# Performance work log

Measured on AMD Instinct MI355X. Metric: run time of the kernel, lower is better.

Reference implementation:

```python
import jax, jax.numpy as jnp
import numpy as np

B, L, D, I = 64, 196, 2048, 512

def setup_inputs() -> dict:
    key = jax.random.key(0)
    ks = jax.random.split(key, 8)
    s_f = 1.0 / np.sqrt(D)
    s_h = 1.0 / np.sqrt(I)
    s_a = 1.0 / np.sqrt(I)
    return {
        "feature_vectors": jax.random.normal(ks[0], (B, L, D), dtype=jnp.float32),
        "hidden_state": jax.random.normal(ks[1], (B, I), dtype=jnp.float32),
        "W_f": jax.random.uniform(ks[2], (D, I), jnp.float32, -s_f, s_f),
        "b_f": jax.random.uniform(ks[3], (I,), jnp.float32, -s_f, s_f),
        "W_h": jax.random.uniform(ks[4], (I, I), jnp.float32, -s_h, s_h),
        "b_h": jax.random.uniform(ks[5], (I,), jnp.float32, -s_h, s_h),
        "W_a": jax.random.uniform(ks[6], (I, D), jnp.float32, -s_a, s_a),
        "b_a": jax.random.uniform(ks[7], (D,), jnp.float32, -s_a, s_a),
    }

def reference(feature_vectors, hidden_state, W_f, b_f, W_h, b_h, W_a, b_a):
    # fv: [B,L,D], hidden: [B,I]
    fv_shaped = jnp.einsum('bld,di->bli', feature_vectors, W_f) + b_f      # [B,L,I]
    hs_shaped = hidden_state @ W_h + b_h                                   # [B,I]
    e = jnp.einsum('bli,id->bld', fv_shaped + hs_shaped[:, None, :], W_a) + b_a  # [B,L,D]
    alpha = jax.nn.softmax(e, axis=1)                                      # softmax over L locations
    z = jnp.sum(alpha * feature_vectors, axis=1)                           # [B,D] (vectorized loop)
    return (z, alpha)
```

## Files before the change

kernel.cpp:

```cpp
#include <hip/hip_runtime.h>

#define B_ 64
#define L_ 196
#define D_ 2048
#define I_ 512
#define M_ (B_*L_)

typedef __attribute__((ext_vector_type(8))) short bf16x8;
typedef __attribute__((ext_vector_type(4))) float f32x4;
typedef unsigned short u16;

__device__ __forceinline__ u16 f2bf(float x){
  unsigned u = __float_as_uint(x);
  u += 0x7fffu + ((u >> 16) & 1u);
  return (u16)(u >> 16);
}

__device__ __forceinline__ void gld16(const void* g, void* l){
  __builtin_amdgcn_global_load_lds(
      (const __attribute__((address_space(1))) void*)g,
      (__attribute__((address_space(3))) void*)l, 16, 0, 0);
}

template<int N> __device__ __forceinline__ void wait_vm(){
  __builtin_amdgcn_s_waitcnt((N&15) | ((N&48)<<10) | (7<<4) | (15<<8));
}
__device__ __forceinline__ void wait_lgkm0(){
  __builtin_amdgcn_s_waitcnt(15 | (48<<10) | (7<<4));
}
__device__ __forceinline__ void bar(){
  asm volatile("" ::: "memory");
  __builtin_amdgcn_s_barrier();
  asm volatile("" ::: "memory");
}

__global__ void transpose_cvt_kernel(const float* __restrict__ in, u16* __restrict__ out, int R, int C){
  __shared__ float tile[32][33];
  int c0 = blockIdx.x*32, r0 = blockIdx.y*32;
  int tx = threadIdx.x, ty = threadIdx.y;
  for (int i=0;i<32;i+=8)
    tile[ty+i][tx] = in[(size_t)(r0+ty+i)*C + c0 + tx];
  __syncthreads();
  for (int i=0;i<32;i+=8)
    out[(size_t)(c0+ty+i)*R + r0 + tx] = f2bf(tile[tx][ty+i]);
}

__launch_bounds__(256)
__global__ void hs_kernel(const float* __restrict__ hidden, const float* __restrict__ Wh,
                          const float* __restrict__ bh, float* __restrict__ hs){
  __shared__ float red[4][64];
  const int nl = threadIdx.x & 63, kg = threadIdx.x >> 6;
  const int n = blockIdx.x*64 + nl, b = blockIdx.y;
  const float* hrow = hidden + b*I_;
  float a0=0.f, a1=0.f;
  #pragma unroll
  for (int k=kg*128; k<kg*128+128; k+=2){
    a0 = fmaf(hrow[k+0], Wh[(size_t)(k+0)*I_ + n], a0);
    a1 = fmaf(hrow[k+1], Wh[(size_t)(k+1)*I_ + n], a1);
  }
  red[kg][nl] = a0 + a1;
  __syncthreads();
  if (kg == 0)
    hs[b*I_ + n] = bh[n] + (red[0][nl]+red[1][nl]) + (red[2][nl]+red[3][nl]);
}

__launch_bounds__(256)
__global__ void gemm1_kernel(const float* __restrict__ A, const u16* __restrict__ Bt,
                             const float* __restrict__ bias, const float* __restrict__ hs,
                             u16* __restrict__ outb)
{
  constexpr int K = D_, BK = 32, NIT = K/BK;
  __shared__ __align__(16) float Als[2][64*32];
  __shared__ __align__(16) u16  Bls[2][64*32];

  const int tid = threadIdx.x, lane = tid&63, wave = tid>>6;
  const int lid = blockIdx.y*8 + blockIdx.x;
  const int wid = (lid & 7)*196 + (lid >> 3);
  const int m0 = (wid >> 3)*64, n0 = (wid & 7)*64;
  const int q = lane>>4, mr = lane&15;
  const int wrow = (wave&1)*32, wcol = (wave>>1)*32;

  const int arow = lane>>3, achk = (lane&7)^arow;
  const float* Ag[2]; int Alo[2];
  #pragma unroll
  for (int u=0;u<2;++u){
    int j = wave*2+u;
    Ag[u] = A + (size_t)(m0 + j*8 + arow)*K + achk*4;
    Alo[u] = j*256;
  }
  const int brow = lane>>2, bchk = (lane&3)^(brow&3);
  const u16* Bg = Bt + (size_t)(n0 + wave*16 + brow)*K + bchk*8;
  const int  Blo = wave*512;

  int afoff[2][2], bgoff[2];
  #pragma unroll
  for (int i2=0;i2<2;i2++)
    #pragma unroll
    for (int p=0;p<2;p++){
      int R = wrow + i2*16 + mr;
      afoff[i2][p] = R*32 + (((2*q+p) ^ (mr&7))*4);
    }
  #pragma unroll
  for (int j=0;j<2;j++){
    int C = wcol + j*16 + mr;
    bgoff[j] = C*32 + ((q ^ (mr&3))*8);
  }

  f32x4 acc[2][2];
  #pragma unroll
  for (int i=0;i<2;i++)
    #pragma unroll
    for (int j=0;j<2;j++) acc[i][j] = (f32x4){0.f,0.f,0.f,0.f};

  #pragma unroll
  for (int u=0;u<2;++u) gld16(Ag[u],    &Als[0][Alo[u]]);
  gld16(Bg,    &Bls[0][Blo]);
  #pragma unroll
  for (int u=0;u<2;++u) gld16(Ag[u]+BK, &Als[1][Alo[u]]);
  gld16(Bg+BK, &Bls[1][Blo]);

  for (int it=0; it<NIT; ++it){
    if (it+1<NIT) wait_vm<3>(); else wait_vm<0>();
    bar();
    const float* Ab = Als[it&1];
    const u16*   Bb = Bls[it&1];
    f32x4 a0[2], a1[2]; bf16x8 bg[2];
    #pragma unroll
    for (int i2=0;i2<2;i2++){
      a0[i2] = *(const f32x4*)(Ab + afoff[i2][0]);
      a1[i2] = *(const f32x4*)(Ab + afoff[i2][1]);
    }
    #pragma unroll
    for (int j=0;j<2;j++) bg[j] = *(const bf16x8*)(Bb + bgoff[j]);
    wait_lgkm0();
    bar();
    if (it+2<NIT){
      int k0 = (it+2)*BK;
      #pragma unroll
      for (int u=0;u<2;++u) gld16(Ag[u]+k0, &Als[it&1][Alo[u]]);
      gld16(Bg+k0, &Bls[it&1][Blo]);
    }
    bf16x8 af[2];
    #pragma unroll
    for (int i2=0;i2<2;i2++){
      #pragma unroll
      for (int e=0;e<4;e++){
        af[i2][e]   = (short)f2bf(a0[i2][e]);
        af[i2][4+e] = (short)f2bf(a1[i2][e]);
      }
    }
    #pragma unroll
    for (int i2=0;i2<2;i2++)
      #pragma unroll
      for (int j=0;j<2;j++)
        acc[i2][j] = __builtin_amdgcn_mfma_f32_16x16x32_bf16(af[i2], bg[j], acc[i2][j], 0,0,0);
  }

  #pragma unroll
  for (int i2=0;i2<2;i2++){
    #pragma unroll
    for (int j=0;j<2;j++){
      int gcol = n0 + wcol + j*16 + mr;
      float bcol = bias[gcol];
      #pragma unroll
      for (int r=0;r<4;r++){
        int grow = m0 + wrow + i2*16 + q*4 + r;
        int batch = grow / L_;
        outb[(size_t)grow*I_ + gcol] = f2bf(acc[i2][j][r] + bcol + hs[batch*I_ + gcol]);
      }
    }
  }
}

__launch_bounds__(256)
__global__ void gemm2_fused_kernel(const u16* __restrict__ T, const u16* __restrict__ Wa,
                                   const float* __restrict__ b_a, const float* __restrict__ fv,
                                   float* __restrict__ out)
{
  constexpr int K = I_, BK = 32, NIT = K/BK;
  __shared__ __align__(16) u16 Als[2][256*32];
  __shared__ __align__(16) u16 Bls[2][64*32];

  const int tid = threadIdx.x, lane = tid&63, wave = tid>>6;
  const int b = blockIdx.y, n0 = blockIdx.x*64;
  const int q = lane>>4, mr = lane&15;
  const int l16 = lane>>2, kc4 = (lane&3)^(l16&3);

  const u16* Ag[4]; int Alo[4];
  #pragma unroll
  for (int u=0;u<4;++u){
    int j = wave*4+u;
    int grow = b*L_ + j*16 + l16; if (grow > M_-1) grow = M_-1;
    Ag[u] = T + (size_t)grow*K + kc4*8; Alo[u] = j*512;
  }
  const u16* Bg = Wa + (size_t)(n0 + wave*16 + l16)*K + kc4*8;
  const int  Blo = wave*512;

  const int abase = mr*32 + ((q ^ (mr&3))*8);
  const int col  = n0 + wave*16 + mr;
  const int boff = (wave*16+mr)*32 + ((q ^ (mr&3))*8);

  f32x4 acc[13];
  #pragma unroll
  for (int i=0;i<13;i++) acc[i] = (f32x4){0,0,0,0};

  #pragma unroll
  for (int u=0;u<4;++u) gld16(Ag[u],    &Als[0][Alo[u]]);
  gld16(Bg,    &Bls[0][Blo]);
  #pragma unroll
  for (int u=0;u<4;++u) gld16(Ag[u]+BK, &Als[1][Alo[u]]);
  gld16(Bg+BK, &Bls[1][Blo]);

  for (int it=0; it<NIT; ++it){
    if (it+1<NIT) wait_vm<5>(); else wait_vm<0>();
    bar();
    const u16* Ab = Als[it&1];
    const u16* Bb = Bls[it&1];
    bf16x8 bg0 = *(const bf16x8*)(Bb + boff);
    bf16x8 af[13];
    #pragma unroll
    for (int i=0;i<13;++i) af[i] = *(const bf16x8*)(Ab + abase + i*512);
    wait_lgkm0();
    bar();
    if (it+2<NIT){
      int k0 = (it+2)*BK;
      #pragma unroll
      for (int u=0;u<4;++u) gld16(Ag[u]+k0, &Als[it&1][Alo[u]]);
      gld16(Bg+k0, &Bls[it&1][Blo]);
    }
    #pragma unroll
    for (int i=0;i<13;++i)
      acc[i] = __builtin_amdgcn_mfma_f32_16x16x32_bf16(af[i], bg0, acc[i], 0,0,0);
  }

  const bool v12 = (q == 0);
  float bc = b_a[col];
  #pragma unroll
  for (int i=0;i<13;++i)
    #pragma unroll
    for (int r=0;r<4;++r) acc[i][r] += bc;

  float m = -3.4e38f;
  #pragma unroll
  for (int i=0;i<12;++i)
    #pragma unroll
    for (int r=0;r<4;++r) m = fmaxf(m, acc[i][r]);
  if (v12)
    #pragma unroll
    for (int r=0;r<4;++r) m = fmaxf(m, acc[12][r]);
  m = fmaxf(m, __shfl_xor(m, 16));
  m = fmaxf(m, __shfl_xor(m, 32));

  float s = 0.f;
  #pragma unroll
  for (int i=0;i<12;++i)
    #pragma unroll
    for (int r=0;r<4;++r){ float e = __expf(acc[i][r]-m); acc[i][r] = e; s += e; }
  if (v12)
    #pragma unroll
    for (int r=0;r<4;++r){ float e = __expf(acc[12][r]-m); acc[12][r] = e; s += e; }
  s += __shfl_xor(s, 16);
  s += __shfl_xor(s, 32);
  float inv = 1.f/s;

  float* alpha = out + (size_t)B_*D_ + (size_t)b*L_*D_;
  const float* fvb = fv + (size_t)b*L_*D_;
  float z = 0.f;
  #pragma unroll
  for (int i=0;i<13;++i){
    if (i < 12 || v12){
      #pragma unroll
      for (int r=0;r<4;++r){
        int row = i*16 + q*4 + r;
        float a = acc[i][r] * inv;
        alpha[(size_t)row*D_ + col] = a;
        z = fmaf(a, fvb[(size_t)row*D_ + col], z);
      }
    }
  }
  z += __shfl_xor(z, 16);
  z += __shfl_xor(z, 32);
  if (q == 0) out[(size_t)b*D_ + col] = z;
}

extern "C" void kernel_launch(void* const* d_in, const int* in_sizes, int n_in,
                              void* d_out, int out_size, void* d_ws, size_t ws_size,
                              hipStream_t stream){
  (void)in_sizes; (void)n_in; (void)out_size; (void)ws_size;
  const float* fv     = (const float*)d_in[0];
  const float* hidden = (const float*)d_in[1];
  const float* W_f    = (const float*)d_in[2];
  const float* b_f    = (const float*)d_in[3];
  const float* W_h    = (const float*)d_in[4];
  const float* b_h    = (const float*)d_in[5];
  const float* W_a    = (const float*)d_in[6];
  const float* b_a    = (const float*)d_in[7];
  float* out = (float*)d_out;

  char* ws = (char*)d_ws;
  u16*   t_bf  = (u16*)ws;
  u16*   WfT   = (u16*)(ws + 12845056);
  u16*   WaT   = (u16*)(ws + 14942208);
  float* hsbuf = (float*)(ws + 17039360);

  transpose_cvt_kernel<<<dim3(I_/32, D_/32), dim3(32,8), 0, stream>>>(W_f, WfT, D_, I_);
  transpose_cvt_kernel<<<dim3(D_/32, I_/32), dim3(32,8), 0, stream>>>(W_a, WaT, I_, D_);
  hs_kernel<<<dim3(I_/64, B_), 256, 0, stream>>>(hidden, W_h, b_h, hsbuf);

  gemm1_kernel<<<dim3(I_/64, M_/64), 256, 0, stream>>>(fv, WfT, b_f, hsbuf, t_bf);
  gemm2_fused_kernel<<<dim3(D_/64, B_), 256, 0, stream>>>(t_bf, WaT, b_a, fv, out);
}
```

Before: 344.5 us.

## Restructure gemm1: register-staged fp32→bf16 conversion, larger 128x64x64 tiles

gemm1 now loads fp32 A tiles into registers, converts them once to bf16 with packed conversion instructions, and stores bf16 into LDS. Previously every wave loaded fp32 directly into LDS and converted after each LDS read. The block tile grows from 64x64 to 128x64 and BK from 32 to 64, with XOR-swizzled bf16 LDS layouts, which raises MFMA work per barrier and halves A-operand LDS footprint. The trade-off is more registers for staging and the loss of asynchronous global-to-LDS loads, which may reduce latency hiding and occupancy.

```diff
diff --git a/kernel.cpp b/kernel.cpp
--- a/kernel.cpp
+++ b/kernel.cpp
@@ -32,6 +32,12 @@
   asm volatile("" ::: "memory");
   __builtin_amdgcn_s_barrier();
   asm volatile("" ::: "memory");
+}
+
+__device__ __forceinline__ unsigned cvtpk(float a, float b){
+  unsigned r;
+  asm("v_cvt_pk_bf16_f32 %0, %1, %2" : "=v"(r) : "v"(a), "v"(b));
+  return r;
 }
 
 __global__ void transpose_cvt_kernel(const float* __restrict__ in, u16* __restrict__ out, int R, int C){
@@ -69,107 +75,118 @@
                              const float* __restrict__ bias, const float* __restrict__ hs,
                              u16* __restrict__ outb)
 {
-  constexpr int K = D_, BK = 32, NIT = K/BK;
-  __shared__ __align__(16) float Als[2][64*32];
-  __shared__ __align__(16) u16  Bls[2][64*32];
+  constexpr int K = D_, BK = 64, NIT = K/BK;
+  __shared__ __align__(16) u16 Als[2][128*64];
+  __shared__ __align__(16) u16 Bls[2][64*64];
 
   const int tid = threadIdx.x, lane = tid&63, wave = tid>>6;
   const int lid = blockIdx.y*8 + blockIdx.x;
-  const int wid = (lid & 7)*196 + (lid >> 3);
-  const int m0 = (wid >> 3)*64, n0 = (wid & 7)*64;
+  const int wid = (lid & 7)*98 + (lid >> 3);
+  const int m0 = (wid >> 3)*128, n0 = (wid & 7)*64;
   const int q = lane>>4, mr = lane&15;
-  const int wrow = (wave&1)*32, wcol = (wave>>1)*32;
-
-  const int arow = lane>>3, achk = (lane&7)^arow;
-  const float* Ag[2]; int Alo[2];
-  #pragma unroll
-  for (int u=0;u<2;++u){
-    int j = wave*2+u;
-    Ag[u] = A + (size_t)(m0 + j*8 + arow)*K + achk*4;
-    Alo[u] = j*256;
-  }
-  const int brow = lane>>2, bchk = (lane&3)^(brow&3);
-  const u16* Bg = Bt + (size_t)(n0 + wave*16 + brow)*K + bchk*8;
-  const int  Blo = wave*512;
-
-  int afoff[2][2], bgoff[2];
-  #pragma unroll
-  for (int i2=0;i2<2;i2++)
-    #pragma unroll
-    for (int p=0;p<2;p++){
-      int R = wrow + i2*16 + mr;
-      afoff[i2][p] = R*32 + (((2*q+p) ^ (mr&7))*4);
-    }
-  #pragma unroll
-  for (int j=0;j<2;j++){
-    int C = wcol + j*16 + mr;
-    bgoff[j] = C*32 + ((q ^ (mr&3))*8);
-  }
-
-  f32x4 acc[2][2];
-  #pragma unroll
-  for (int i=0;i<2;i++)
-    #pragma unroll
-    for (int j=0;j<2;j++) acc[i][j] = (f32x4){0.f,0.f,0.f,0.f};
-
-  #pragma unroll
-  for (int u=0;u<2;++u) gld16(Ag[u],    &Als[0][Alo[u]]);
-  gld16(Bg,    &Bls[0][Blo]);
-  #pragma unroll
-  for (int u=0;u<2;++u) gld16(Ag[u]+BK, &Als[1][Alo[u]]);
-  gld16(Bg+BK, &Bls[1][Blo]);
-
-  for (int it=0; it<NIT; ++it){
-    if (it+1<NIT) wait_vm<3>(); else wait_vm<0>();
-    bar();
-    const float* Ab = Als[it&1];
-    const u16*   Bb = Bls[it&1];
-    f32x4 a0[2], a1[2]; bf16x8 bg[2];
-    #pragma unroll
-    for (int i2=0;i2<2;i2++){
-      a0[i2] = *(const f32x4*)(Ab + afoff[i2][0]);
-      a1[i2] = *(const f32x4*)(Ab + afoff[i2][1]);
-    }
-    #pragma unroll
-    for (int j=0;j<2;j++) bg[j] = *(const bf16x8*)(Bb + bgoff[j]);
+  const int wm = (wave&1)*64, wn = (wave>>1)*32;
+
+  const int a_r  = wave*32 + (lane>>4);
+  const int a_kc = lane&15;
+  const float* Aw = A + (size_t)(m0 + a_r)*K + a_kc*4;
+  const int b_r  = wave*16 + (lane>>3);
+  const int b_kc = lane&7;
+  const u16* Bw = Bt + (size_t)(n0 + b_r)*K + b_kc*8;
+
+  int awo[8], bwo[2];
+  #pragma unroll
+  for (int u=0;u<8;++u){
+    int r = a_r + u*4;
+    awo[u] = r*64 + (((a_kc>>1) ^ (r&7))*8) + (a_kc&1)*4;
+  }
+  #pragma unroll
+  for (int v=0;v<2;++v){
+    int r = b_r + v*8;
+    bwo[v] = r*64 + ((b_kc ^ (r&7))*8);
+  }
+
+  int aro[2][4], bro[2][2];
+  #pragma unroll
+  for (int s=0;s<2;++s){
+    #pragma unroll
+    for (int i2=0;i2<4;++i2){
+      int r = wm + i2*16 + mr;
+      aro[s][i2] = r*64 + (((s*4+q) ^ (r&7))*8);
+    }
+    #pragma unroll
+    for (int j=0;j<2;++j){
+      int r = wn + j*16 + mr;
+      bro[s][j] = r*64 + (((s*4+q) ^ (r&7))*8);
+    }
+  }
+
+  f32x4 rA[8]; bf16x8 rB[2];
+  f32x4 acc[4][2];
+  #pragma unroll
+  for (int i=0;i<4;++i)
+    #pragma unroll
+    for (int j=0;j<2;++j) acc[i][j] = (f32x4){0.f,0.f,0.f,0.f};
+
+#define G1_LOAD(k0) { \
+  _Pragma("unroll") \
+  for (int u=0;u<8;++u) rA[u] = *(const f32x4*)(Aw + (size_t)(u*4)*K + (k0)); \
+  _Pragma("unroll") \
+  for (int v=0;v<2;++v) rB[v] = *(const bf16x8*)(Bw + (size_t)(v*8)*K + (k0)); }
+
+#define G1_CVTWR(bi) { \
+  u16* Ab_ = Als[bi]; u16* Bb_ = Bls[bi]; \
+  _Pragma("unroll") \
+  for (int u=0;u<8;++u){ \
+    unsigned lo = cvtpk(rA[u][0], rA[u][1]); \
+    unsigned hi = cvtpk(rA[u][2], rA[u][3]); \
+    *(uint2*)(Ab_ + awo[u]) = make_uint2(lo, hi); \
+  } \
+  _Pragma("unroll") \
+  for (int v=0;v<2;++v) *(bf16x8*)(Bb_ + bwo[v]) = rB[v]; }
+
+  G1_LOAD(0)
+  G1_CVTWR(0)
+  G1_LOAD(BK)
+  wait_lgkm0(); bar();
+
+  for (int t=0; t<NIT; ++t){
+    if (t+1 < NIT) G1_CVTWR((t+1)&1)
+    if (t+2 < NIT) G1_LOAD((t+2)*BK)
+    const u16* Ab = Als[t&1];
+    const u16* Bb = Bls[t&1];
+    #pragma unroll
+    for (int s=0;s<2;++s){
+      bf16x8 af[4], bg[2];
+      #pragma unroll
+      for (int i2=0;i2<4;++i2) af[i2] = *(const bf16x8*)(Ab + aro[s][i2]);
+      #pragma unroll
+      for (int j=0;j<2;++j)    bg[j]  = *(const bf16x8*)(Bb + bro[s][j]);
+      #pragma unroll
+      for (int i2=0;i2<4;++i2)
+        #pragma unroll
+        for (int j=0;j<2;++j)
+          acc[i2][j] = __builtin_amdgcn_mfma_f32_16x16x32_bf16(af[i2], bg[j], acc[i2][j], 0,0,0);
+    }
     wait_lgkm0();
     bar();
-    if (it+2<NIT){
-      int k0 = (it+2)*BK;
-      #pragma unroll
-      for (int u=0;u<2;++u) gld16(Ag[u]+k0, &Als[it&1][Alo[u]]);
-      gld16(Bg+k0, &Bls[it&1][Blo]);
-    }
-    bf16x8 af[2];
-    #pragma unroll
-    for (int i2=0;i2<2;i2++){
-      #pragma unroll
-      for (int e=0;e<4;e++){
-        af[i2][e]   = (short)f2bf(a0[i2][e]);
-        af[i2][4+e] = (short)f2bf(a1[i2][e]);
-      }
-    }
-    #pragma unroll
-    for (int i2=0;i2<2;i2++)
-      #pragma unroll
-      for (int j=0;j<2;j++)
-        acc[i2][j] = __builtin_amdgcn_mfma_f32_16x16x32_bf16(af[i2], bg[j], acc[i2][j], 0,0,0);
-  }
-
-  #pragma unroll
-  for (int i2=0;i2<2;i2++){
-    #pragma unroll
-    for (int j=0;j<2;j++){
-      int gcol = n0 + wcol + j*16 + mr;
+  }
+
+  #pragma unroll
+  for (int i2=0;i2<4;++i2){
+    #pragma unroll
+    for (int j=0;j<2;++j){
+      int gcol = n0 + wn + j*16 + mr;
       float bcol = bias[gcol];
       #pragma unroll
-      for (int r=0;r<4;r++){
-        int grow = m0 + wrow + i2*16 + q*4 + r;
+      for (int r=0;r<4;++r){
+        int grow = m0 + wm + i2*16 + q*4 + r;
         int batch = grow / L_;
         outb[(size_t)grow*I_ + gcol] = f2bf(acc[i2][j][r] + bcol + hs[batch*I_ + gcol]);
       }
     }
   }
+#undef G1_LOAD
+#undef G1_CVTWR
 }
 
 __launch_bounds__(256)
@@ -307,6 +324,6 @@
   transpose_cvt_kernel<<<dim3(D_/32, I_/32), dim3(32,8), 0, stream>>>(W_a, WaT, I_, D_);
   hs_kernel<<<dim3(I_/64, B_), 256, 0, stream>>>(hidden, W_h, b_h, hsbuf);
 
-  gemm1_kernel<<<dim3(I_/64, M_/64), 256, 0, stream>>>(fv, WfT, b_f, hsbuf, t_bf);
+  gemm1_kernel<<<dim3(8, M_/128), 256, 0, stream>>>(fv, WfT, b_f, hsbuf, t_bf);
   gemm2_fused_kernel<<<dim3(D_/64, B_), 256, 0, stream>>>(t_bf, WaT, b_a, fv, out);
 }
```

Result: faster. 313.1 us (-9.1%).
